# Kernel optimization log

Hardware: AMD Instinct MI355X
Metric: run time of the kernel (lower is better)

Reference implementation:

```python
import jax, jax.numpy as jnp
import numpy as np

N_NODES = 50000
N_EDGES = 800000
N_GRAPHS = 64
NEG_SLOPE = 0.2  # PyG GATv2Conv default negative_slope
LN_EPS = 1e-5


def gatv2(x, src, dst, Wl, bl, Wr, br, att, bias, heads, out_ch, concat):
    """Faithful eval-mode PyG GATv2Conv: x_l=lin_l(x) (source), x_r=lin_r(x) (target),
    e = att . leaky_relu(x_l[src] + x_r[dst]), segment-softmax over dst, scatter-add."""
    N = x.shape[0]
    H, C = heads, out_ch
    xl = (x @ Wl + bl).reshape(N, H, C)
    xr = (x @ Wr + br).reshape(N, H, C)
    e = jax.nn.leaky_relu(xl[src] + xr[dst], NEG_SLOPE)        # [E, H, C]
    logits = jnp.einsum('ehc,hc->eh', e, att)                  # [E, H]
    m = jax.ops.segment_max(logits, dst, num_segments=N)       # every node has a self-loop
    ex = jnp.exp(logits - m[dst])
    denom = jax.ops.segment_sum(ex, dst, num_segments=N)
    alpha = ex / (denom[dst] + 1e-16)                          # [E, H]
    out = jax.ops.segment_sum(xl[src] * alpha[..., None], dst, num_segments=N)  # [N, H, C]
    out = out.reshape(N, H * C) if concat else out.mean(axis=1)
    return out + bias


def setup_inputs() -> dict:
    key = jax.random.key(0)
    ks = jax.random.split(key, 32)

    def g(i, shape):  # glorot-ish
        scale = np.sqrt(2.0 / (shape[0] + shape[-1]))
        return (jax.random.normal(ks[i], shape, jnp.float32) * scale)

    inp = {
        'x': jax.random.normal(ks[0], (N_NODES, 4), jnp.float32),
        'edge_index': jax.random.randint(ks[1], (2, N_EDGES), 0, N_NODES, dtype=jnp.int64),
        'batch': jnp.sort(jax.random.randint(ks[2], (N_NODES,), 0, N_GRAPHS, dtype=jnp.int64)),
        # conv1: 4 -> 64, heads=4, concat -> 256
        'W1l': g(3, (4, 256)), 'b1l': jnp.zeros((256,), jnp.float32),
        'W1r': g(4, (4, 256)), 'b1r': jnp.zeros((256,), jnp.float32),
        'a1': g(5, (4, 64)), 'c1b': jnp.zeros((256,), jnp.float32),
        # conv2: 256 -> 64, heads=2, concat -> 128
        'W2l': g(6, (256, 128)), 'b2l': jnp.zeros((128,), jnp.float32),
        'W2r': g(7, (256, 128)), 'b2r': jnp.zeros((128,), jnp.float32),
        'a2': g(8, (2, 64)), 'c2b': jnp.zeros((128,), jnp.float32),
        # conv3: 128 -> 256, heads=1, concat=False -> 256
        'W3l': g(9, (128, 256)), 'b3l': jnp.zeros((256,), jnp.float32),
        'W3r': g(10, (128, 256)), 'b3r': jnp.zeros((256,), jnp.float32),
        'a3': g(11, (1, 256)), 'c3b': jnp.zeros((256,), jnp.float32),
        # enhancer MLP + LayerNorm
        'We1': g(12, (256, 512)), 'be1': jnp.zeros((512,), jnp.float32),
        'We2': g(13, (512, 256)), 'be2': jnp.zeros((256,), jnp.float32),
        'lng': jnp.ones((256,), jnp.float32), 'lnb': jnp.zeros((256,), jnp.float32),
    }
    return inp


def reference(x, edge_index, batch,
              W1l, b1l, W1r, b1r, a1, c1b,
              W2l, b2l, W2r, b2r, a2, c2b,
              W3l, b3l, W3r, b3r, a3, c3b,
              We1, be1, We2, be2, lng, lnb):
    N = x.shape[0]
    loop = jnp.arange(N, dtype=edge_index.dtype)  # add_self_loops=True (PyG default)
    src = jnp.concatenate([edge_index[0], loop])
    dst = jnp.concatenate([edge_index[1], loop])

    h = jax.nn.relu(gatv2(x, src, dst, W1l, b1l, W1r, b1r, a1, c1b, 4, 64, True))
    h = jax.nn.relu(gatv2(h, src, dst, W2l, b2l, W2r, b2r, a2, c2b, 2, 64, True))
    h = gatv2(h, src, dst, W3l, b3l, W3r, b3r, a3, c3b, 1, 256, False)

    # global mean pool per graph
    sums = jax.ops.segment_sum(h, batch, num_segments=N_GRAPHS)          # [G, 256]
    cnt = jax.ops.segment_sum(jnp.ones((N, 1), h.dtype), batch, num_segments=N_GRAPHS)
    pooled = sums / jnp.maximum(cnt, 1.0)

    # enhancer (dropout off in eval): Linear -> ReLU -> Linear -> LayerNorm
    z = jax.nn.relu(pooled @ We1 + be1) @ We2 + be2
    mu = z.mean(axis=-1, keepdims=True)
    var = z.var(axis=-1, keepdims=True)
    return (z - mu) / jnp.sqrt(var + LN_EPS) * lng + lnb
```

## Files before the change

kernel.cpp:

```cpp
#include <hip/hip_runtime.h>
#include <hip/hip_bf16.h>
#include <math.h>

#define NN 50000
#define NE0 800000
#define ETOT (NE0 + NN)
#define NG 64
#define SCAN_BLKS ((NN + 63) / 64)
#define DMAX_THR 8.0f

typedef _Float16 h2 __attribute__((ext_vector_type(2)));
typedef _Float16 h8 __attribute__((ext_vector_type(8)));
typedef float    f32x4 __attribute__((ext_vector_type(4)));

__device__ __forceinline__ unsigned short f2h(float f) {
    _Float16 h = (_Float16)f;
    return __builtin_bit_cast(unsigned short, h);
}

__device__ __forceinline__ void edge_sd(const int* __restrict__ ei, int e, int& s, int& d) {
    if (e < NE0) { s = ei[e]; d = ei[NE0 + e]; }
    else { s = e - NE0; d = s; }
}

__global__ __launch_bounds__(256)
void hist_dst(const int* __restrict__ ei, int* __restrict__ deg) {
    int e = blockIdx.x * blockDim.x + threadIdx.x;
    if (e >= ETOT) return;
    int s, d; edge_sd(ei, e, s, d); (void)s;
    atomicAdd(&deg[d], 1);
}

__global__ __launch_bounds__(64)
void scan1(const int* __restrict__ deg, int* __restrict__ psum) {
    int i = blockIdx.x * 64 + threadIdx.x;
    int v = (i < NN) ? deg[i] : 0;
#pragma unroll
    for (int off = 1; off < 64; off <<= 1) {
        int t = __shfl_up(v, off);
        if ((int)threadIdx.x >= off) v += t;
    }
    if (threadIdx.x == 63) psum[blockIdx.x] = v;
}

__global__ __launch_bounds__(1024)
void scan2(int* __restrict__ psum) {
    __shared__ int sm[1024];
    int t = threadIdx.x;
    sm[t] = (t < SCAN_BLKS) ? psum[t] : 0;
    __syncthreads();
    for (int off = 1; off < 1024; off <<= 1) {
        int v = (t >= off) ? sm[t - off] : 0;
        __syncthreads();
        sm[t] += v;
        __syncthreads();
    }
    if (t < SCAN_BLKS) psum[t] = (t == 0) ? 0 : sm[t - 1];
}

__global__ __launch_bounds__(64)
void scan3(const int* __restrict__ deg, const int* __restrict__ psum,
           int* __restrict__ rowptr, int* __restrict__ cursor) {
    int i = blockIdx.x * 64 + threadIdx.x;
    int v = (i < NN) ? deg[i] : 0;
    int inc = v;
#pragma unroll
    for (int off = 1; off < 64; off <<= 1) {
        int t = __shfl_up(inc, off);
        if ((int)threadIdx.x >= off) inc += t;
    }
    int excl = inc - v + psum[blockIdx.x];
    if (i < NN) { rowptr[i] = excl; cursor[i] = excl; }
    if (i == NN - 1) rowptr[NN] = excl + v;
}

__global__ __launch_bounds__(256)
void scatter_csr(const int* __restrict__ ei, int* __restrict__ cursor,
                 int* __restrict__ col) {
    int e = blockIdx.x * blockDim.x + threadIdx.x;
    if (e >= ETOT) return;
    int s, d; edge_sd(ei, e, s, d);
    int pos = atomicAdd(&cursor[d], 1);
    col[pos] = s;
}

__device__ __forceinline__ void wfrag_one(const float* W, unsigned short* Wf,
                                          int r, int KB, int NOUT) {
    int j = r & 7;
    int l = (r >> 3) & 63;
    int rest = r >> 9;
    int kb = rest % KB, t = rest / KB;
    int k = kb * 32 + (l >> 4) * 8 + j;
    int colj = t * 16 + (l & 15);
    Wf[r] = f2h(W[(size_t)k * NOUT + colj]);
}
__global__ __launch_bounds__(256)
void wfrag_all(const float* __restrict__ W2l, const float* __restrict__ W2r,
               const float* __restrict__ W3l, const float* __restrict__ W3r,
               unsigned short* __restrict__ Wf2l, unsigned short* __restrict__ Wf2r,
               unsigned short* __restrict__ Wf3l, unsigned short* __restrict__ Wf3r) {
    int tid = blockIdx.x * 256 + threadIdx.x;
    int seg = tid >> 15;
    int r = tid & 32767;
    if (seg == 0)      wfrag_one(W2l, Wf2l, r, 8, 128);
    else if (seg == 1) wfrag_one(W2r, Wf2r, r, 8, 128);
    else if (seg == 2) wfrag_one(W3l, Wf3l, r, 4, 256);
    else               wfrag_one(W3r, Wf3r, r, 4, 256);
}

__global__ __launch_bounds__(256)
void blr_prep(const float* __restrict__ X, const float* __restrict__ W1r,
              const float* __restrict__ b1r, const float* __restrict__ b1l,
              float* __restrict__ out) {
    int j = blockIdx.x * 64 + (threadIdx.x & 63);
    int row0 = (blockIdx.y * 4 + (threadIdx.x >> 6)) * 8;
    float w0 = W1r[j], w1 = W1r[256 + j], w2 = W1r[512 + j], w3 = W1r[768 + j];
    float bj = b1r[j] + b1l[j];
#pragma unroll
    for (int r = 0; r < 8; ++r) {
        int row = row0 + r;
        if (row >= NN) break;
        float4 xv = *reinterpret_cast<const float4*>(X + (size_t)row * 4);
        out[(size_t)row * 256 + j] =
            fmaf(xv.x, w0, fmaf(xv.y, w1, fmaf(xv.z, w2, fmaf(xv.w, w3, bj))));
    }
}

__global__ __launch_bounds__(256)
void gat1_fused(const float* __restrict__ x,
                const int* __restrict__ rowptr, const int* __restrict__ col,
                const float* __restrict__ BLR,
                const float* __restrict__ W1l, const float* __restrict__ b1l,
                const float* __restrict__ a1, const float* __restrict__ c1b,
                unsigned short* __restrict__ out) {
    int lane = threadIdx.x & 63;
    int node = (blockIdx.x * blockDim.x + threadIdx.x) >> 6;
    if (node >= NN) return;
    int ch0 = lane * 4;

    float wl[4][4];
#pragma unroll
    for (int k = 0; k < 4; ++k) {
        float4 l4 = *reinterpret_cast<const float4*>(W1l + k * 256 + ch0);
        wl[k][0] = l4.x; wl[k][1] = l4.y; wl[k][2] = l4.z; wl[k][3] = l4.w;
    }
    float4 av  = *reinterpret_cast<const float4*>(a1 + ch0);
    float ar[4] = { av.x, av.y, av.z, av.w };
    float4 blv = *reinterpret_cast<const float4*>(b1l + ch0);
    float4 cbv = *reinterpret_cast<const float4*>(c1b + ch0);
    float obias[4] = { blv.x + cbv.x, blv.y + cbv.y, blv.z + cbv.z, blv.w + cbv.w };

    const float4* x4 = reinterpret_cast<const float4*>(x);

    float4 blrv = *reinterpret_cast<const float4*>(BLR + (size_t)node * 256 + ch0);
    float blr[4] = { blrv.x, blrv.y, blrv.z, blrv.w };

    float m = -INFINITY, l = 0.f;
    float ax = 0.f, ay = 0.f, az = 0.f, aw = 0.f;

    int beg = rowptr[node], end = rowptr[node + 1];
    int idx = beg;
    for (; idx + 3 < end; idx += 4) {
        float4 v[4];
        float dd[4];
#pragma unroll
        for (int q = 0; q < 4; ++q) v[q] = x4[col[idx + q]];
#pragma unroll
        for (int q = 0; q < 4; ++q) {
            float d = 0.f;
#pragma unroll
            for (int p = 0; p < 4; ++p) {
                float u = fmaf(v[q].x, wl[0][p], fmaf(v[q].y, wl[1][p],
                          fmaf(v[q].z, wl[2][p], fmaf(v[q].w, wl[3][p], blr[p]))));
                u = u > 0.f ? u : 0.2f * u;
                d = fmaf(u, ar[p], d);
            }
            dd[q] = d;
        }
#pragma unroll
        for (int off = 8; off >= 1; off >>= 1) {
#pragma unroll
            for (int q = 0; q < 4; ++q) dd[q] += __shfl_xor(dd[q], off);
        }
        float pmax = fmaxf(fmaxf(dd[0], dd[1]), fmaxf(dd[2], dd[3]));
        if (pmax > m + DMAX_THR) {
            float sc = __expf(m - pmax);
            l *= sc; ax *= sc; ay *= sc; az *= sc; aw *= sc;
            m = pmax;
        }
        float p0 = __expf(dd[0] - m), p1 = __expf(dd[1] - m);
        float p2 = __expf(dd[2] - m), p3 = __expf(dd[3] - m);
        l += (p0 + p1) + (p2 + p3);
        ax += fmaf(p0, v[0].x, p1 * v[1].x) + fmaf(p2, v[2].x, p3 * v[3].x);
        ay += fmaf(p0, v[0].y, p1 * v[1].y) + fmaf(p2, v[2].y, p3 * v[3].y);
        az += fmaf(p0, v[0].z, p1 * v[1].z) + fmaf(p2, v[2].z, p3 * v[3].z);
        aw += fmaf(p0, v[0].w, p1 * v[1].w) + fmaf(p2, v[2].w, p3 * v[3].w);
    }
    for (; idx < end; ++idx) {
        float4 v0 = x4[col[idx]];
        float d0 = 0.f;
#pragma unroll
        for (int p = 0; p < 4; ++p) {
            float u0 = fmaf(v0.x, wl[0][p], fmaf(v0.y, wl[1][p],
                       fmaf(v0.z, wl[2][p], fmaf(v0.w, wl[3][p], blr[p]))));
            u0 = u0 > 0.f ? u0 : 0.2f * u0;
            d0 = fmaf(u0, ar[p], d0);
        }
#pragma unroll
        for (int off = 8; off >= 1; off >>= 1) d0 += __shfl_xor(d0, off);
        if (d0 > m + DMAX_THR) {
            float sc = __expf(m - d0);
            l *= sc; ax *= sc; ay *= sc; az *= sc; aw *= sc;
            m = d0;
        }
        float p0 = __expf(d0 - m);
        l += p0;
        ax = fmaf(p0, v0.x, ax);
        ay = fmaf(p0, v0.y, ay);
        az = fmaf(p0, v0.z, az);
        aw = fmaf(p0, v0.w, aw);
    }
    float inv = 1.f / (l + 1e-16f);
    unsigned short o[4];
#pragma unroll
    for (int p = 0; p < 4; ++p) {
        float v = fmaf(ax, wl[0][p], fmaf(ay, wl[1][p],
                  fmaf(az, wl[2][p], aw * wl[3][p]))) * inv + obias[p];
        o[p] = f2h(fmaxf(v, 0.f));
    }
    *reinterpret_cast<ushort4*>(out + (size_t)node * 256 + ch0) =
        make_ushort4(o[0], o[1], o[2], o[3]);
}

template<int KIN, int NOUT>
__global__ __launch_bounds__(256)
void gemm_mfma2(const unsigned short* __restrict__ X,
                const unsigned short* __restrict__ WfL, const float* __restrict__ bL,
                unsigned short* __restrict__ outL,
                const unsigned short* __restrict__ WfR, const float* __restrict__ bR,
                unsigned short* __restrict__ outR) {
    constexpr int KB = KIN / 32, NT = NOUT / 16;
    int lane = threadIdx.x & 63;
    int wv = threadIdx.x >> 6;
    int row0 = blockIdx.x * 64 + wv * 16;
    int r16 = lane & 15, kg = lane >> 4;

    int arow = row0 + r16; if (arow >= NN) arow = NN - 1;
    const unsigned short* xrow = X + (size_t)arow * KIN + kg * 8;
    h8 af[KB];
#pragma unroll
    for (int kb = 0; kb < KB; ++kb)
        af[kb] = *reinterpret_cast<const h8*>(xrow + kb * 32);

    const unsigned short* Wf[2] = { WfL, WfR };
    const float* bb[2] = { bL, bR };
    unsigned short* oo[2] = { outL, outR };

#pragma unroll
    for (int w = 0; w < 2; ++w) {
        const h8* wbase = reinterpret_cast<const h8*>(Wf[w]) + lane;
        const float* bw = bb[w];
        unsigned short* ow = oo[w];
#pragma unroll 1
        for (int t = 0; t < NT; ++t) {
            f32x4 acc = {0.f, 0.f, 0.f, 0.f};
            const h8* wp = wbase + (size_t)t * KB * 64;
#pragma unroll
            for (int kb = 0; kb < KB; ++kb)
                acc = __builtin_amdgcn_mfma_f32_16x16x32_f16(af[kb], wp[kb * 64], acc, 0, 0, 0);
            float bv = bw[t * 16 + r16];
#pragma unroll
            for (int rg = 0; rg < 4; ++rg) {
                int row = row0 + kg * 4 + rg;
                if (row < NN)
                    ow[(size_t)row * NOUT + t * 16 + r16] = f2h(acc[rg] + bv);
            }
        }
    }
}

__global__ __launch_bounds__(256)
void gat2_fused(const unsigned short* __restrict__ xl, const unsigned short* __restrict__ xr,
                const int* __restrict__ rowptr, const int* __restrict__ col,
                const float* __restrict__ att, const float* __restrict__ bias,
                unsigned short* __restrict__ out) {
    constexpr int HC = 128;
    int lane = threadIdx.x & 63;
    int half = lane >> 5;
    int l32 = lane & 31;
    int node = (blockIdx.x * blockDim.x + threadIdx.x) >> 6;
    if (node >= NN) return;
    int ch0 = l32 * 4;

    const h2 c02 = (h2){(_Float16)0.2f, (_Float16)0.2f};
    h2 a2[2];
#pragma unroll
    for (int p = 0; p < 2; ++p)
        a2[p] = (h2){(_Float16)att[ch0 + 2*p], (_Float16)att[ch0 + 2*p + 1]};
    const h2* xrp = reinterpret_cast<const h2*>(xr + (size_t)node * HC + ch0);
    h2 xr2[2] = { xrp[0], xrp[1] };

    float m = -INFINITY, l = 0.f, acc[4] = {0.f, 0.f, 0.f, 0.f};

    int beg = rowptr[node], end = rowptr[node + 1];
    int n = end - beg;
    int nh = (n + 1) >> 1;
    int idx = beg + (half ? nh : 0);
    int myEnd = half ? end : beg + nh;

    for (; idx + 1 < myEnd; idx += 2) {
        int s0 = col[idx], s1 = col[idx + 1];
        const h2* p0 = reinterpret_cast<const h2*>(xl + (size_t)s0 * HC + ch0);
        const h2* p1 = reinterpret_cast<const h2*>(xl + (size_t)s1 * HC + ch0);
        h2 e0[2] = { p0[0], p0[1] };
        h2 e1[2] = { p1[0], p1[1] };
        float d0 = 0.f, d1 = 0.f;
#pragma unroll
        for (int p = 0; p < 2; ++p) {
            h2 u0 = e0[p] + xr2[p];
            h2 u1 = e1[p] + xr2[p];
            u0 = __builtin_elementwise_max(u0, u0 * c02);
            u1 = __builtin_elementwise_max(u1, u1 * c02);
            d0 = __builtin_amdgcn_fdot2(u0, a2[p], d0, false);
            d1 = __builtin_amdgcn_fdot2(u1, a2[p], d1, false);
        }
#pragma unroll
        for (int off = 8; off >= 1; off >>= 1) {
            d0 += __shfl_xor(d0, off);
            d1 += __shfl_xor(d1, off);
        }
        float pmax = fmaxf(d0, d1);
        if (pmax > m + DMAX_THR) {
            float sc = __expf(m - pmax);
            l *= sc;
#pragma unroll
            for (int p = 0; p < 4; ++p) acc[p] *= sc;
            m = pmax;
        }
        float pw0 = __expf(d0 - m), pw1 = __expf(d1 - m);
        l += pw0 + pw1;
#pragma unroll
        for (int p = 0; p < 4; ++p)
            acc[p] = fmaf(pw0, (float)e0[p >> 1][p & 1],
                     fmaf(pw1, (float)e1[p >> 1][p & 1], acc[p]));
    }
    if (idx < myEnd) {
        int s0 = col[idx];
        const h2* p0 = reinterpret_cast<const h2*>(xl + (size_t)s0 * HC + ch0);
        h2 e0[2] = { p0[0], p0[1] };
        float d0 = 0.f;
#pragma unroll
        for (int p = 0; p < 2; ++p) {
            h2 u0 = e0[p] + xr2[p];
            u0 = __builtin_elementwise_max(u0, u0 * c02);
            d0 = __builtin_amdgcn_fdot2(u0, a2[p], d0, false);
        }
#pragma unroll
        for (int off = 8; off >= 1; off >>= 1) d0 += __shfl_xor(d0, off);
        if (d0 > m + DMAX_THR) {
            float sc = __expf(m - d0);
            l *= sc;
#pragma unroll
            for (int p = 0; p < 4; ++p) acc[p] *= sc;
            m = d0;
        }
        float pw0 = __expf(d0 - m);
        l += pw0;
#pragma unroll
        for (int p = 0; p < 4; ++p)
            acc[p] = fmaf(pw0, (float)e0[p >> 1][p & 1], acc[p]);
    }

    float mo = __shfl_xor(m, 32);
    float lo = __shfl_xor(l, 32);
    float M = fmaxf(m, mo);
    float sA = __expf(m - M), sB = __expf(mo - M);
    float lsum = l * sA + lo * sB;
    float inv = 1.f / (lsum + 1e-16f);
    unsigned short o[4];
#pragma unroll
    for (int p = 0; p < 4; ++p) {
        float ao = __shfl_xor(acc[p], 32);
        float v = (acc[p] * sA + ao * sB) * inv + bias[ch0 + p];
        o[p] = f2h(fmaxf(v, 0.f));
    }
    if (half == 0)
        *reinterpret_cast<ushort4*>(out + (size_t)node * HC + ch0) =
            make_ushort4(o[0], o[1], o[2], o[3]);
}

__global__ __launch_bounds__(256)
void gat3_fused(const unsigned short* __restrict__ xl, const unsigned short* __restrict__ xr,
                const int* __restrict__ rowptr, const int* __restrict__ col,
                const float* __restrict__ att, const float* __restrict__ bias,
                float* __restrict__ out) {
    int lane = threadIdx.x & 63;
    int half = lane >> 5;
    int node = (blockIdx.x * blockDim.x + threadIdx.x) >> 6;
    if (node >= NN) return;
    int ch0 = (lane & 31) * 8;

    const h2 c02 = (h2){(_Float16)0.2f, (_Float16)0.2f};
    h2 a2[4];
#pragma unroll
    for (int p = 0; p < 4; ++p)
        a2[p] = (h2){(_Float16)att[ch0 + 2*p], (_Float16)att[ch0 + 2*p + 1]};
    const h2* xrp = reinterpret_cast<const h2*>(xr + (size_t)node * 256 + ch0);
    h2 xr2[4] = { xrp[0], xrp[1], xrp[2], xrp[3] };

    float m = -INFINITY, l = 0.f, acc[8];
#pragma unroll
    for (int p = 0; p < 8; ++p) acc[p] = 0.f;

    int beg = rowptr[node], end = rowptr[node + 1];
    int n = end - beg;
    int nh = (n + 1) >> 1;
    int idx = beg + (half ? nh : 0);
    int myEnd = half ? end : beg + nh;

    for (; idx + 1 < myEnd; idx += 2) {
        int s0 = col[idx], s1 = col[idx + 1];
        const h2* p0 = reinterpret_cast<const h2*>(xl + (size_t)s0 * 256 + ch0);
        const h2* p1 = reinterpret_cast<const h2*>(xl + (size_t)s1 * 256 + ch0);
        h2 e0[4] = { p0[0], p0[1], p0[2], p0[3] };
        h2 e1[4] = { p1[0], p1[1], p1[2], p1[3] };
        float d0 = 0.f, d1 = 0.f;
#pragma unroll
        for (int p = 0; p < 4; ++p) {
            h2 u0 = e0[p] + xr2[p];
            h2 u1 = e1[p] + xr2[p];
            u0 = __builtin_elementwise_max(u0, u0 * c02);
            u1 = __builtin_elementwise_max(u1, u1 * c02);
            d0 = __builtin_amdgcn_fdot2(u0, a2[p], d0, false);
            d1 = __builtin_amdgcn_fdot2(u1, a2[p], d1, false);
        }
#pragma unroll
        for (int off = 16; off >= 1; off >>= 1) {
            d0 += __shfl_xor(d0, off);
            d1 += __shfl_xor(d1, off);
        }
        float pmax = fmaxf(d0, d1);
        if (pmax > m + DMAX_THR) {
            float sc = __expf(m - pmax);
            l *= sc;
#pragma unroll
            for (int p = 0; p < 8; ++p) acc[p] *= sc;
            m = pmax;
        }
        float pw0 = __expf(d0 - m), pw1 = __expf(d1 - m);
        l += pw0 + pw1;
#pragma unroll
        for (int p = 0; p < 8; ++p)
            acc[p] = fmaf(pw0, (float)e0[p >> 1][p & 1],
                     fmaf(pw1, (float)e1[p >> 1][p & 1], acc[p]));
    }
    if (idx < myEnd) {
        int s0 = col[idx];
        const h2* p0 = reinterpret_cast<const h2*>(xl + (size_t)s0 * 256 + ch0);
        h2 e0[4] = { p0[0], p0[1], p0[2], p0[3] };
        float d0 = 0.f;
#pragma unroll
        for (int p = 0; p < 4; ++p) {
            h2 u0 = e0[p] + xr2[p];
            u0 = __builtin_elementwise_max(u0, u0 * c02);
            d0 = __builtin_amdgcn_fdot2(u0, a2[p], d0, false);
        }
#pragma unroll
        for (int off = 16; off >= 1; off >>= 1) d0 += __shfl_xor(d0, off);
        if (d0 > m + DMAX_THR) {
            float sc = __expf(m - d0);
            l *= sc;
#pragma unroll
            for (int p = 0; p < 8; ++p) acc[p] *= sc;
            m = d0;
        }
        float pw0 = __expf(d0 - m);
        l += pw0;
#pragma unroll
        for (int p = 0; p < 8; ++p)
            acc[p] = fmaf(pw0, (float)e0[p >> 1][p & 1], acc[p]);
    }

    float mo = __shfl_xor(m, 32);
    float lo = __shfl_xor(l, 32);
    float M = fmaxf(m, mo);
    float sA = __expf(m - M), sB = __expf(mo - M);
    float lsum = l * sA + lo * sB;
    float inv = 1.f / (lsum + 1e-16f);
    float o[8];
#pragma unroll
    for (int p = 0; p < 8; ++p) {
        float ao = __shfl_xor(acc[p], 32);
        o[p] = (acc[p] * sA + ao * sB) * inv + bias[ch0 + p];
    }
    if (half == 0) {
        *reinterpret_cast<float4*>(out + (size_t)node * 256 + ch0) =
            make_float4(o[0], o[1], o[2], o[3]);
        *reinterpret_cast<float4*>(out + (size_t)node * 256 + ch0 + 4) =
            make_float4(o[4], o[5], o[6], o[7]);
    }
}

__global__ __launch_bounds__(256)
void graph_bounds(const int* __restrict__ batch, float* __restrict__ cnt,
                  float* __restrict__ pooled) {
    int g = blockIdx.x, tid = threadIdx.x;
    pooled[g * 256 + tid] = 0.f;
    if (tid == 0) {
        int lo = 0, hi = NN;
        while (lo < hi) { int mid = (lo + hi) >> 1; if (batch[mid] < g) lo = mid + 1; else hi = mid; }
        int lo2 = lo, hi2 = NN;
        while (lo2 < hi2) { int mid = (lo2 + hi2) >> 1; if (batch[mid] < g + 1) lo2 = mid + 1; else hi2 = mid; }
        cnt[g] = (float)(lo2 - lo);
    }
}

__global__ __launch_bounds__(256)
void pool_sum(const float* __restrict__ h, const int* __restrict__ batch,
              float* pooled) {
    __shared__ int gb[32];
    int c = threadIdx.x;
    int n0 = blockIdx.x * 32;
    int n1 = min(n0 + 32, NN);
    int cnt = n1 - n0;
    if (c < cnt) gb[c] = batch[n0 + c];
    __syncthreads();
    if (gb[0] == gb[cnt - 1]) {
        float acc = 0.f;
#pragma unroll 4
        for (int i = 0; i < cnt; ++i) acc += h[(size_t)(n0 + i) * 256 + c];
        atomicAdd(&pooled[gb[0] * 256 + c], acc);
    } else {
        int cur = gb[0]; float acc = 0.f;
        for (int i = 0; i < cnt; ++i) {
            int g = gb[i];
            if (g != cur) { atomicAdd(&pooled[cur * 256 + c], acc); acc = 0.f; cur = g; }
            acc += h[(size_t)(n0 + i) * 256 + c];
        }
        atomicAdd(&pooled[cur * 256 + c], acc);
    }
}

__global__ __launch_bounds__(256)
void mlp_ln(const float* __restrict__ pooled, const float* __restrict__ cnt,
            const float* __restrict__ We1, const float* __restrict__ be1,
            const float* __restrict__ We2, const float* __restrict__ be2,
            const float* __restrict__ lng, const float* __restrict__ lnb,
            float* __restrict__ out) {
    __shared__ float p[256];
    __shared__ float t[512];
    __shared__ float red[8];
    int g = blockIdx.x, tid = threadIdx.x;
    p[tid] = pooled[g * 256 + tid] / fmaxf(cnt[g], 1.0f);
    __syncthreads();
    for (int jj = tid; jj < 512; jj += 256) {
        float s = be1[jj];
        for (int k = 0; k < 256; ++k) s = fmaf(p[k], We1[(size_t)k * 512 + jj], s);
        t[jj] = fmaxf(s, 0.f);
    }
    __syncthreads();
    float z = be2[tid];
    for (int k = 0; k < 512; ++k) z = fmaf(t[k], We2[(size_t)k * 256 + tid], z);
    float sv = z, sq = z * z;
#pragma unroll
    for (int off = 32; off >= 1; off >>= 1) {
        sv += __shfl_xor(sv, off);
        sq += __shfl_xor(sq, off);
    }
    int wv = tid >> 6;
    if ((tid & 63) == 0) { red[wv] = sv; red[4 + wv] = sq; }
    __syncthreads();
    float tot = red[0] + red[1] + red[2] + red[3];
    float totq = red[4] + red[5] + red[6] + red[7];
    float mu = tot * (1.f / 256.f);
    float var = totq * (1.f / 256.f) - mu * mu;
    float r = rsqrtf(var + 1e-5f);
    out[g * 256 + tid] = (z - mu) * r * lng[tid] + lnb[tid];
}

extern "C" void kernel_launch(void* const* d_in, const int* in_sizes, int n_in,
                              void* d_out, int out_size, void* d_ws, size_t ws_size,
                              hipStream_t stream) {
    const float* x   = (const float*)d_in[0];
    const int*   ei  = (const int*)d_in[1];
    const int*   bat = (const int*)d_in[2];
    const float *W1l = (const float*)d_in[3], *b1l = (const float*)d_in[4];
    const float *W1r = (const float*)d_in[5], *b1r = (const float*)d_in[6];
    const float *a1  = (const float*)d_in[7], *c1b = (const float*)d_in[8];
    const float *W2l = (const float*)d_in[9],  *b2l = (const float*)d_in[10];
    const float *W2r = (const float*)d_in[11], *b2r = (const float*)d_in[12];
    const float *a2  = (const float*)d_in[13], *c2b = (const float*)d_in[14];
    const float *W3l = (const float*)d_in[15], *b3l = (const float*)d_in[16];
    const float *W3r = (const float*)d_in[17], *b3r = (const float*)d_in[18];
    const float *a3  = (const float*)d_in[19], *c3b = (const float*)d_in[20];
    const float *We1 = (const float*)d_in[21], *be1 = (const float*)d_in[22];
    const float *We2 = (const float*)d_in[23], *be2 = (const float*)d_in[24];
    const float *lng = (const float*)d_in[25], *lnb = (const float*)d_in[26];

    char* base = (char*)d_ws;
    size_t off = 0;
    auto nxt = [&](size_t bytes) { char* p = base + off; off = (off + bytes + 255) & ~(size_t)255; return p; };
    unsigned short* Abuf = (unsigned short*)nxt((size_t)NN * 256 * 2);
    unsigned short* Bbuf = (unsigned short*)nxt((size_t)NN * 256 * 2);
    unsigned short* Hb16 = (unsigned short*)nxt((size_t)NN * 256 * 2);
    float* Hb32 = (float*)nxt((size_t)NN * 256 * 4);
    float* BLR  = (float*)nxt((size_t)NN * 256 * 4);
    int* deg    = (int*)nxt(NN * 4);
    int* rowptr = (int*)nxt((NN + 1) * 4);
    int* cursor = (int*)nxt(NN * 4);
    int* colv   = (int*)nxt((size_t)ETOT * 4);
    int* psum   = (int*)nxt(1024 * 4);
    float* POOL = (float*)nxt(NG * 256 * 4);
    float* CNT  = (float*)nxt(NG * 4);
    unsigned short* Wf2l = (unsigned short*)nxt(256 * 128 * 2);
    unsigned short* Wf2r = (unsigned short*)nxt(256 * 128 * 2);
    unsigned short* Wf3l = (unsigned short*)nxt(128 * 256 * 2);
    unsigned short* Wf3r = (unsigned short*)nxt(128 * 256 * 2);

    const int GEMM_BLKS = (NN + 63) / 64;
    const int NB_NODE = (NN + 3) / 4;

    hipMemsetAsync(deg, 0, NN * sizeof(int), stream);
    hist_dst<<<(ETOT + 255) / 256, 256, 0, stream>>>(ei, deg);
    scan1<<<SCAN_BLKS, 64, 0, stream>>>(deg, psum);
    scan2<<<1, 1024, 0, stream>>>(psum);
    scan3<<<SCAN_BLKS, 64, 0, stream>>>(deg, psum, rowptr, cursor);
    scatter_csr<<<(ETOT + 255) / 256, 256, 0, stream>>>(ei, cursor, colv);

    wfrag_all<<<(4 * 32768) / 256, 256, 0, stream>>>(W2l, W2r, W3l, W3r, Wf2l, Wf2r, Wf3l, Wf3r);
    {
        dim3 g(4, (NN + 31) / 32);
        blr_prep<<<g, 256, 0, stream>>>(x, W1r, b1r, b1l, BLR);
    }

    gat1_fused<<<NB_NODE, 256, 0, stream>>>(x, rowptr, colv, BLR, W1l, b1l, a1, c1b, Hb16);

    gemm_mfma2<256, 128><<<GEMM_BLKS, 256, 0, stream>>>(Hb16, Wf2l, b2l, Abuf, Wf2r, b2r, Bbuf);
    gat2_fused<<<NB_NODE, 256, 0, stream>>>(Abuf, Bbuf, rowptr, colv, a2, c2b, Hb16);

    gemm_mfma2<128, 256><<<GEMM_BLKS, 256, 0, stream>>>(Hb16, Wf3l, b3l, Abuf, Wf3r, b3r, Bbuf);
    gat3_fused<<<NB_NODE, 256, 0, stream>>>(Abuf, Bbuf, rowptr, colv, a3, c3b, Hb32);

    graph_bounds<<<NG, 256, 0, stream>>>(bat, CNT, POOL);
    pool_sum<<<(NN + 31) / 32, 256, 0, stream>>>(Hb32, bat, POOL);
    mlp_ln<<<NG, 256, 0, stream>>>(POOL, CNT, We1, be1, We2, be2, lng, lnb, (float*)d_out);
}
```

Baseline: 441.1 us.

## Precompute fp16 layer-1 source/target projections and split edges across half-waves

Layer 1 no longer gathers the 4-wide raw features and recomputes the 4x256 projection on every edge. A prep kernel now writes fp16 tables of x@W1l+b1l and x@W1r+b1r, and the attention kernel gathers 512-byte fp16 rows using packed half math and fdot2. Each wave's two halves process alternate halves of a node's edge list, then merge their online-softmax states with cross-half shuffles. This trades per-edge ALU work for much larger gathered reads (512 B per edge instead of 16 B) and an extra 50 MB of table writes, and fp16 logits may reduce accuracy.

```diff
diff --git a/kernel.cpp b/kernel.cpp
--- a/kernel.cpp
+++ b/kernel.cpp
@@ -12,6 +12,7 @@
 typedef _Float16 h2 __attribute__((ext_vector_type(2)));
 typedef _Float16 h8 __attribute__((ext_vector_type(8)));
 typedef float    f32x4 __attribute__((ext_vector_type(4)));
+typedef unsigned short us8 __attribute__((ext_vector_type(8)));
 
 __device__ __forceinline__ unsigned short f2h(float f) {
     _Float16 h = (_Float16)f;
@@ -109,127 +110,134 @@
 }
 
 __global__ __launch_bounds__(256)
-void blr_prep(const float* __restrict__ X, const float* __restrict__ W1r,
-              const float* __restrict__ b1r, const float* __restrict__ b1l,
-              float* __restrict__ out) {
+void qr_prep(const float* __restrict__ X,
+             const float* __restrict__ W1l, const float* __restrict__ b1l,
+             const float* __restrict__ W1r, const float* __restrict__ b1r,
+             unsigned short* __restrict__ Q, unsigned short* __restrict__ R) {
     int j = blockIdx.x * 64 + (threadIdx.x & 63);
     int row0 = (blockIdx.y * 4 + (threadIdx.x >> 6)) * 8;
-    float w0 = W1r[j], w1 = W1r[256 + j], w2 = W1r[512 + j], w3 = W1r[768 + j];
-    float bj = b1r[j] + b1l[j];
+    float l0 = W1l[j], l1 = W1l[256 + j], l2 = W1l[512 + j], l3 = W1l[768 + j];
+    float r0 = W1r[j], r1 = W1r[256 + j], r2 = W1r[512 + j], r3 = W1r[768 + j];
+    float bl = b1l[j], br = b1r[j];
 #pragma unroll
     for (int r = 0; r < 8; ++r) {
         int row = row0 + r;
         if (row >= NN) break;
         float4 xv = *reinterpret_cast<const float4*>(X + (size_t)row * 4);
-        out[(size_t)row * 256 + j] =
-            fmaf(xv.x, w0, fmaf(xv.y, w1, fmaf(xv.z, w2, fmaf(xv.w, w3, bj))));
-    }
-}
-
-__global__ __launch_bounds__(256)
-void gat1_fused(const float* __restrict__ x,
+        float q = fmaf(xv.x, l0, fmaf(xv.y, l1, fmaf(xv.z, l2, fmaf(xv.w, l3, bl))));
+        float rr = fmaf(xv.x, r0, fmaf(xv.y, r1, fmaf(xv.z, r2, fmaf(xv.w, r3, br))));
+        Q[(size_t)row * 256 + j] = f2h(q);
+        R[(size_t)row * 256 + j] = f2h(rr);
+    }
+}
+
+__global__ __launch_bounds__(256)
+void gat1_fused(const unsigned short* __restrict__ Q, const unsigned short* __restrict__ R,
                 const int* __restrict__ rowptr, const int* __restrict__ col,
-                const float* __restrict__ BLR,
-                const float* __restrict__ W1l, const float* __restrict__ b1l,
-                const float* __restrict__ a1, const float* __restrict__ c1b,
+                const float* __restrict__ att, const float* __restrict__ bias,
                 unsigned short* __restrict__ out) {
     int lane = threadIdx.x & 63;
+    int half = lane >> 5;
     int node = (blockIdx.x * blockDim.x + threadIdx.x) >> 6;
     if (node >= NN) return;
-    int ch0 = lane * 4;
-
-    float wl[4][4];
-#pragma unroll
-    for (int k = 0; k < 4; ++k) {
-        float4 l4 = *reinterpret_cast<const float4*>(W1l + k * 256 + ch0);
-        wl[k][0] = l4.x; wl[k][1] = l4.y; wl[k][2] = l4.z; wl[k][3] = l4.w;
-    }
-    float4 av  = *reinterpret_cast<const float4*>(a1 + ch0);
-    float ar[4] = { av.x, av.y, av.z, av.w };
-    float4 blv = *reinterpret_cast<const float4*>(b1l + ch0);
-    float4 cbv = *reinterpret_cast<const float4*>(c1b + ch0);
-    float obias[4] = { blv.x + cbv.x, blv.y + cbv.y, blv.z + cbv.z, blv.w + cbv.w };
-
-    const float4* x4 = reinterpret_cast<const float4*>(x);
-
-    float4 blrv = *reinterpret_cast<const float4*>(BLR + (size_t)node * 256 + ch0);
-    float blr[4] = { blrv.x, blrv.y, blrv.z, blrv.w };
-
-    float m = -INFINITY, l = 0.f;
-    float ax = 0.f, ay = 0.f, az = 0.f, aw = 0.f;
+    int ch0 = (lane & 31) * 8;
+
+    const h2 c02 = (h2){(_Float16)0.2f, (_Float16)0.2f};
+    h2 a2[4];
+#pragma unroll
+    for (int p = 0; p < 4; ++p)
+        a2[p] = (h2){(_Float16)att[ch0 + 2*p], (_Float16)att[ch0 + 2*p + 1]};
+    const h2* rp = reinterpret_cast<const h2*>(R + (size_t)node * 256 + ch0);
+    h2 r2[4] = { rp[0], rp[1], rp[2], rp[3] };
+
+    float m = -INFINITY, l = 0.f, acc[8];
+#pragma unroll
+    for (int p = 0; p < 8; ++p) acc[p] = 0.f;
 
     int beg = rowptr[node], end = rowptr[node + 1];
-    int idx = beg;
-    for (; idx + 3 < end; idx += 4) {
-        float4 v[4];
-        float dd[4];
-#pragma unroll
-        for (int q = 0; q < 4; ++q) v[q] = x4[col[idx + q]];
-#pragma unroll
-        for (int q = 0; q < 4; ++q) {
-            float d = 0.f;
-#pragma unroll
-            for (int p = 0; p < 4; ++p) {
-                float u = fmaf(v[q].x, wl[0][p], fmaf(v[q].y, wl[1][p],
-                          fmaf(v[q].z, wl[2][p], fmaf(v[q].w, wl[3][p], blr[p]))));
-                u = u > 0.f ? u : 0.2f * u;
-                d = fmaf(u, ar[p], d);
-            }
-            dd[q] = d;
-        }
-#pragma unroll
-        for (int off = 8; off >= 1; off >>= 1) {
-#pragma unroll
-            for (int q = 0; q < 4; ++q) dd[q] += __shfl_xor(dd[q], off);
-        }
-        float pmax = fmaxf(fmaxf(dd[0], dd[1]), fmaxf(dd[2], dd[3]));
+    int n = end - beg;
+    int nh = (n + 1) >> 1;
+    int idx = beg + (half ? nh : 0);
+    int myEnd = half ? end : beg + nh;
+
+    for (; idx + 1 < myEnd; idx += 2) {
+        int s0 = col[idx], s1 = col[idx + 1];
+        const h2* p0 = reinterpret_cast<const h2*>(Q + (size_t)s0 * 256 + ch0);
+        const h2* p1 = reinterpret_cast<const h2*>(Q + (size_t)s1 * 256 + ch0);
+        h2 e0[4] = { p0[0], p0[1], p0[2], p0[3] };
+        h2 e1[4] = { p1[0], p1[1], p1[2], p1[3] };
+        float d0 = 0.f, d1 = 0.f;
+#pragma unroll
+        for (int p = 0; p < 4; ++p) {
+            h2 u0 = e0[p] + r2[p];
+            h2 u1 = e1[p] + r2[p];
+            u0 = __builtin_elementwise_max(u0, u0 * c02);
+            u1 = __builtin_elementwise_max(u1, u1 * c02);
+            d0 = __builtin_amdgcn_fdot2(u0, a2[p], d0, false);
+            d1 = __builtin_amdgcn_fdot2(u1, a2[p], d1, false);
+        }
+#pragma unroll
+        for (int off = 4; off >= 1; off >>= 1) {
+            d0 += __shfl_xor(d0, off);
+            d1 += __shfl_xor(d1, off);
+        }
+        float pmax = fmaxf(d0, d1);
         if (pmax > m + DMAX_THR) {
             float sc = __expf(m - pmax);
-            l *= sc; ax *= sc; ay *= sc; az *= sc; aw *= sc;
+            l *= sc;
+#pragma unroll
+            for (int p = 0; p < 8; ++p) acc[p] *= sc;
             m = pmax;
         }
-        float p0 = __expf(dd[0] - m), p1 = __expf(dd[1] - m);
-        float p2 = __expf(dd[2] - m), p3 = __expf(dd[3] - m);
-        l += (p0 + p1) + (p2 + p3);
-        ax += fmaf(p0, v[0].x, p1 * v[1].x) + fmaf(p2, v[2].x, p3 * v[3].x);
-        ay += fmaf(p0, v[0].y, p1 * v[1].y) + fmaf(p2, v[2].y, p3 * v[3].y);
-        az += fmaf(p0, v[0].z, p1 * v[1].z) + fmaf(p2, v[2].z, p3 * v[3].z);
-        aw += fmaf(p0, v[0].w, p1 * v[1].w) + fmaf(p2, v[2].w, p3 * v[3].w);
-    }
-    for (; idx < end; ++idx) {
-        float4 v0 = x4[col[idx]];
+        float pw0 = __expf(d0 - m), pw1 = __expf(d1 - m);
+        l += pw0 + pw1;
+#pragma unroll
+        for (int p = 0; p < 8; ++p)
+            acc[p] = fmaf(pw0, (float)e0[p >> 1][p & 1],
+                     fmaf(pw1, (float)e1[p >> 1][p & 1], acc[p]));
+    }
+    if (idx < myEnd) {
+        int s0 = col[idx];
+        const h2* p0 = reinterpret_cast<const h2*>(Q + (size_t)s0 * 256 + ch0);
+        h2 e0[4] = { p0[0], p0[1], p0[2], p0[3] };
         float d0 = 0.f;
 #pragma unroll
         for (int p = 0; p < 4; ++p) {
-            float u0 = fmaf(v0.x, wl[0][p], fmaf(v0.y, wl[1][p],
-                       fmaf(v0.z, wl[2][p], fmaf(v0.w, wl[3][p], blr[p]))));
-            u0 = u0 > 0.f ? u0 : 0.2f * u0;
-            d0 = fmaf(u0, ar[p], d0);
-        }
-#pragma unroll
-        for (int off = 8; off >= 1; off >>= 1) d0 += __shfl_xor(d0, off);
+            h2 u0 = e0[p] + r2[p];
+            u0 = __builtin_elementwise_max(u0, u0 * c02);
+            d0 = __builtin_amdgcn_fdot2(u0, a2[p], d0, false);
+        }
+#pragma unroll
+        for (int off = 4; off >= 1; off >>= 1) d0 += __shfl_xor(d0, off);
         if (d0 > m + DMAX_THR) {
             float sc = __expf(m - d0);
-            l *= sc; ax *= sc; ay *= sc; az *= sc; aw *= sc;
+            l *= sc;
+#pragma unroll
+            for (int p = 0; p < 8; ++p) acc[p] *= sc;
             m = d0;
         }
-        float p0 = __expf(d0 - m);
-        l += p0;
-        ax = fmaf(p0, v0.x, ax);
-        ay = fmaf(p0, v0.y, ay);
-        az = fmaf(p0, v0.z, az);
-        aw = fmaf(p0, v0.w, aw);
-    }
-    float inv = 1.f / (l + 1e-16f);
-    unsigned short o[4];
-#pragma unroll
-    for (int p = 0; p < 4; ++p) {
-        float v = fmaf(ax, wl[0][p], fmaf(ay, wl[1][p],
-                  fmaf(az, wl[2][p], aw * wl[3][p]))) * inv + obias[p];
+        float pw0 = __expf(d0 - m);
+        l += pw0;
+#pragma unroll
+        for (int p = 0; p < 8; ++p)
+            acc[p] = fmaf(pw0, (float)e0[p >> 1][p & 1], acc[p]);
+    }
+
+    float mo = __shfl_xor(m, 32);
+    float lo = __shfl_xor(l, 32);
+    float M = fmaxf(m, mo);
+    float sA = __expf(m - M), sB = __expf(mo - M);
+    float lsum = l * sA + lo * sB;
+    float inv = 1.f / (lsum + 1e-16f);
+    us8 o;
+#pragma unroll
+    for (int p = 0; p < 8; ++p) {
+        float ao = __shfl_xor(acc[p], 32);
+        float v = (acc[p] * sA + ao * sB) * inv + bias[ch0 + p];
         o[p] = f2h(fmaxf(v, 0.f));
     }
-    *reinterpret_cast<ushort4*>(out + (size_t)node * 256 + ch0) =
-        make_ushort4(o[0], o[1], o[2], o[3]);
+    if (half == 0)
+        *reinterpret_cast<us8*>(out + (size_t)node * 256 + ch0) = o;
 }
 
 template<int KIN, int NOUT>
@@ -604,7 +612,8 @@
     unsigned short* Bbuf = (unsigned short*)nxt((size_t)NN * 256 * 2);
     unsigned short* Hb16 = (unsigned short*)nxt((size_t)NN * 256 * 2);
     float* Hb32 = (float*)nxt((size_t)NN * 256 * 4);
-    float* BLR  = (float*)nxt((size_t)NN * 256 * 4);
+    unsigned short* Qtab = (unsigned short*)nxt((size_t)NN * 256 * 2);
+    unsigned short* Rtab = (unsigned short*)nxt((size_t)NN * 256 * 2);
     int* deg    = (int*)nxt(NN * 4);
     int* rowptr = (int*)nxt((NN + 1) * 4);
     int* cursor = (int*)nxt(NN * 4);
@@ -630,10 +639,10 @@
     wfrag_all<<<(4 * 32768) / 256, 256, 0, stream>>>(W2l, W2r, W3l, W3r, Wf2l, Wf2r, Wf3l, Wf3r);
     {
         dim3 g(4, (NN + 31) / 32);
-        blr_prep<<<g, 256, 0, stream>>>(x, W1r, b1r, b1l, BLR);
-    }
-
-    gat1_fused<<<NB_NODE, 256, 0, stream>>>(x, rowptr, colv, BLR, W1l, b1l, a1, c1b, Hb16);
+        qr_prep<<<g, 256, 0, stream>>>(x, W1l, b1l, W1r, b1r, Qtab, Rtab);
+    }
+
+    gat1_fused<<<NB_NODE, 256, 0, stream>>>(Qtab, Rtab, rowptr, colv, a1, c1b, Hb16);
 
     gemm_mfma2<256, 128><<<GEMM_BLKS, 256, 0, stream>>>(Hb16, Wf2l, b2l, Abuf, Wf2r, b2r, Bbuf);
     gat2_fused<<<NB_NODE, 256, 0, stream>>>(Abuf, Bbuf, rowptr, colv, a2, c2b, Hb16);
```

Result: faster. 416.7 us (-5.5%).
